# Performance work log

Measured on AMD Instinct MI355X. Metric: run time of the kernel, lower is better.

Reference implementation:

```python
import jax, jax.numpy as jnp
import numpy as np

B, N, C, H = 8, 1024, 768, 12
D = C // H  # 64


def setup_inputs() -> dict:
    key = jax.random.key(0)
    ks = jax.random.split(key, 6)
    x = jax.random.normal(ks[0], (B, N, C), dtype=jnp.float32)
    pad_mask = jnp.ones((B, N), dtype=jnp.int32)
    # params (torch Linear stored transposed; here kept as (in, out) for x @ W)
    s = 1.0 / np.sqrt(C)
    w_attn = jax.random.uniform(ks[1], (C, 3 * C), jnp.float32, -s, s)
    b_attn = jax.random.uniform(ks[2], (3 * C,), jnp.float32, -s, s)
    w_proj = jax.random.uniform(ks[3], (C, C), jnp.float32, -s, s)
    b_proj = jax.random.uniform(ks[4], (C,), jnp.float32, -s, s)
    return {"x": x, "pad_mask": pad_mask, "w_attn": w_attn,
            "b_attn": b_attn, "w_proj": w_proj, "b_proj": b_proj}


def reference(x, pad_mask, w_attn, b_attn, w_proj, b_proj):
    # qkv projection
    qkv = x @ w_attn + b_attn                      # [B,N,3C]
    q, k, v = jnp.split(qkv, 3, axis=-1)
    q = q.reshape(B, N, H, D).transpose(0, 2, 1, 3)  # [B,H,N,D]
    k = k.reshape(B, N, H, D).transpose(0, 2, 1, 3)
    v = v.reshape(B, N, H, D).transpose(0, 2, 1, 3)
    scale = 1.0 / np.sqrt(D)
    att = jnp.einsum('bhqd,bhkd->bhqk', q, k) * scale  # [B,H,N,N]
    # NOTE: original code's causal masked_fill is non-in-place and discarded,
    # so the causal mask is NOT applied. Only the pad mask (over query rows) is.
    pm = pad_mask.reshape(B, 1, N, 1)
    att = jnp.where(pm == 0, -jnp.inf, att)
    att = jax.nn.softmax(att, axis=-1)
    out = jnp.einsum('bhqk,bhkd->bhqd', att, v)     # [B,H,N,D]
    out = out.transpose(0, 2, 1, 3).reshape(B, N, C)
    # dropout layers are identity in eval mode
    return out @ w_proj + b_proj
```

## Files before the change

### kernel.cpp

```cpp
#include <hip/hip_runtime.h>
#include <hip/hip_bf16.h>

#define B_  8
#define N_  1024
#define C_  768
#define H_  12
#define D_  64
#define C3  2304
#define C2  1536

typedef unsigned short ushort_t;
typedef __attribute__((ext_vector_type(8))) short bf16x8;
typedef __attribute__((ext_vector_type(4))) float f32x4;

__device__ __forceinline__ float bf2f(ushort_t u) {
    union { unsigned int i; float f; } v;
    v.i = ((unsigned int)u) << 16;
    return v.f;
}

__device__ __forceinline__ ushort_t f2bf(float f) {
    union { float f; unsigned int i; } v;
    v.f = f;
    unsigned int x = v.i;
    if ((x & 0x7f800000u) == 0x7f800000u && (x & 0x007fffffu))
        return (ushort_t)((x >> 16) | 0x0040u);
    return (ushort_t)((x + 0x7fffu + ((x >> 16) & 1u)) >> 16);
}

__device__ __forceinline__ void st1(float* p, float v) { *p = v; }
__device__ __forceinline__ void st1(ushort_t* p, float v) { *p = f2bf(v); }

__global__ __launch_bounds__(256) void cvt_bf16(
    const float* __restrict__ X, ushort_t* __restrict__ Y, int n)
{
    int i = (blockIdx.x * 256 + threadIdx.x) * 4;
    if (i < n) {
        float4 f = *reinterpret_cast<const float4*>(X + i);
        ushort4 o;
        o.x = f2bf(f.x); o.y = f2bf(f.y); o.z = f2bf(f.z); o.w = f2bf(f.w);
        *reinterpret_cast<ushort4*>(Y + i) = o;
    }
}

__global__ __launch_bounds__(256) void transpose_to_bf16(
    const float* __restrict__ W, ushort_t* __restrict__ WT, int K, int Nn)
{
    __shared__ float t[32][33];
    const int n0 = blockIdx.x * 32, k0 = blockIdx.y * 32;
    const int tx = threadIdx.x & 31, ty = threadIdx.x >> 5;
    #pragma unroll
    for (int i = 0; i < 4; ++i) {
        const int k = ty + i * 8;
        t[k][tx] = W[(size_t)(k0 + k) * Nn + n0 + tx];
    }
    __syncthreads();
    #pragma unroll
    for (int i = 0; i < 4; ++i) {
        const int n = ty + i * 8;
        WT[(size_t)(n0 + n) * K + k0 + tx] = f2bf(t[tx][n]);
    }
}

__device__ __forceinline__ void gld_lds16(const ushort_t* g, ushort_t* lds) {
    __builtin_amdgcn_global_load_lds(
        (const __attribute__((address_space(1))) void*)g,
        (__attribute__((address_space(3))) void*)lds, 16, 0, 0);
}

template<typename TO, bool SCALEQ>
__global__ __launch_bounds__(256) void gemm_mfma(
    const ushort_t* __restrict__ A, const ushort_t* __restrict__ BT,
    const float* __restrict__ bias, TO* __restrict__ Y, int ldY,
    ushort_t* __restrict__ vtOut, int M, int K, int Nn)
{
    __shared__ ushort_t As[128 * 32];
    __shared__ ushort_t Bs[128 * 32];

    const int tid  = threadIdx.x;
    const int wave = tid >> 6;
    const int lane = tid & 63;
    const int row0 = blockIdx.y * 128;
    const int col0 = blockIdx.x * 128;
    const int wr   = (wave >> 1) * 64;
    const int wc   = (wave & 1) * 64;
    const int l15  = lane & 15;
    const int quad = lane >> 4;

    const int lrow = lane >> 2;
    const int sk   = (lane & 3) * 8;

    f32x4 acc[4][4] = {};

    for (int k0 = 0; k0 < K; k0 += 32) {
        __syncthreads();
        #pragma unroll
        for (int it = 0; it < 2; ++it) {
            const int baseRow = it * 64 + wave * 16;
            const int r = baseRow + lrow;
            gld_lds16(&A [(size_t)(row0 + r) * K + k0 + sk], &As[baseRow * 32]);
            gld_lds16(&BT[(size_t)(col0 + r) * K + k0 + sk], &Bs[baseRow * 32]);
        }
        __syncthreads();

        bf16x8 af[4], bf[4];
        #pragma unroll
        for (int i = 0; i < 4; ++i) {
            af[i] = *reinterpret_cast<const bf16x8*>(&As[(wr + i * 16 + l15) * 32 + quad * 8]);
            bf[i] = *reinterpret_cast<const bf16x8*>(&Bs[(wc + i * 16 + l15) * 32 + quad * 8]);
        }
        #pragma unroll
        for (int i = 0; i < 4; ++i)
            #pragma unroll
            for (int j = 0; j < 4; ++j)
                acc[i][j] = __builtin_amdgcn_mfma_f32_16x16x32_bf16(
                    af[i], bf[j], acc[i][j], 0, 0, 0);
    }

    const float qs = (SCALEQ && (col0 + wc) < C_) ? 0.125f : 1.0f;

    if (vtOut != nullptr && col0 >= C2) {
        #pragma unroll
        for (int i = 0; i < 4; ++i) {
            const int r0 = row0 + wr + i * 16 + quad * 4;
            const int bb = r0 >> 10;
            const int n  = r0 & 1023;
            #pragma unroll
            for (int j = 0; j < 4; ++j) {
                const int c  = col0 + wc + j * 16 + l15;
                const int cv = c - C2;
                const int hh = cv >> 6, d = cv & 63;
                const float bv = bias[c];
                ushort4 o;
                o.x = f2bf(acc[i][j][0] + bv);
                o.y = f2bf(acc[i][j][1] + bv);
                o.z = f2bf(acc[i][j][2] + bv);
                o.w = f2bf(acc[i][j][3] + bv);
                *reinterpret_cast<ushort4*>(
                    &vtOut[((size_t)(bb * H_ + hh) * D_ + d) * N_ + n]) = o;
            }
        }
    } else {
        #pragma unroll
        for (int i = 0; i < 4; ++i) {
            const int r = row0 + wr + i * 16 + quad * 4;
            #pragma unroll
            for (int j = 0; j < 4; ++j) {
                const int c = col0 + wc + j * 16 + l15;
                const float bv = bias[c];
                #pragma unroll
                for (int t = 0; t < 4; ++t)
                    st1(&Y[(size_t)(r + t) * ldY + c], (acc[i][j][t] + bv) * qs);
            }
        }
    }
}

#define LDT 72

__global__ __launch_bounds__(256) void attn_mfma(
    const ushort_t* __restrict__ qk, const ushort_t* __restrict__ vt,
    const int* __restrict__ pad_mask, ushort_t* __restrict__ y)
{
    __shared__ ushort_t Ks [64 * LDT];
    __shared__ ushort_t Vts[64 * LDT];
    __shared__ ushort_t Ps [4][32 * LDT];

    const int tid  = threadIdx.x;
    const int wave = tid >> 6;
    const int lane = tid & 63;
    const int l15  = lane & 15;
    const int quad = lane >> 4;

    const int qt = blockIdx.x & 7;
    const int h  = (blockIdx.x >> 3) % H_;
    const int b  = blockIdx.x / (8 * H_);
    const int q0 = qt * 128 + wave * 32;

    const ushort_t* qkB = qk + (size_t)b * N_ * C2;
    const ushort_t* vtB = vt + ((size_t)(b * H_ + h)) * D_ * N_;
    const int ho = h * D_;

    bf16x8 qf[2][2];
    #pragma unroll
    for (int rt = 0; rt < 2; ++rt)
        #pragma unroll
        for (int kc = 0; kc < 2; ++kc)
            qf[rt][kc] = *reinterpret_cast<const bf16x8*>(
                &qkB[(size_t)(q0 + rt * 16 + l15) * C2 + ho + kc * 32 + quad * 8]);

    int mrow[2][4];
    #pragma unroll
    for (int rt = 0; rt < 2; ++rt)
        #pragma unroll
        for (int t = 0; t < 4; ++t)
            mrow[rt][t] = pad_mask[b * N_ + q0 + rt * 16 + quad * 4 + t];

    f32x4 oacc[2][4] = {};
    float den[2][4] = {};

    const int srow = tid >> 3;
    const int scol = (tid & 7) * 8;

    for (int k0 = 0; k0 < N_; k0 += 64) {
        __syncthreads();
        #pragma unroll
        for (int half = 0; half < 2; ++half) {
            const int r = srow + half * 32;
            uint4 kv = *reinterpret_cast<const uint4*>(
                &qkB[(size_t)(k0 + r) * C2 + C_ + ho + scol]);
            uint4 vv = *reinterpret_cast<const uint4*>(
                &vtB[(size_t)r * N_ + k0 + scol]);
            *reinterpret_cast<uint4*>(&Ks [r * LDT + scol]) = kv;
            *reinterpret_cast<uint4*>(&Vts[r * LDT + scol]) = vv;
        }
        __syncthreads();

        f32x4 s[2][4] = {};
        #pragma unroll
        for (int kc = 0; kc < 2; ++kc) {
            bf16x8 kf[4];
            #pragma unroll
            for (int ct = 0; ct < 4; ++ct)
                kf[ct] = *reinterpret_cast<const bf16x8*>(
                    &Ks[(ct * 16 + l15) * LDT + kc * 32 + quad * 8]);
            #pragma unroll
            for (int rt = 0; rt < 2; ++rt)
                #pragma unroll
                for (int ct = 0; ct < 4; ++ct)
                    s[rt][ct] = __builtin_amdgcn_mfma_f32_16x16x32_bf16(
                        qf[rt][kc], kf[ct], s[rt][ct], 0, 0, 0);
        }

        ushort_t* Pw = Ps[wave];
        #pragma unroll
        for (int rt = 0; rt < 2; ++rt)
            #pragma unroll
            for (int ct = 0; ct < 4; ++ct)
                #pragma unroll
                for (int t = 0; t < 4; ++t) {
                    float p = __expf(s[rt][ct][t]);
                    unsigned u = (__float_as_uint(p) + 0x8000u) & 0xffff0000u;
                    den[rt][t] += __uint_as_float(u);
                    Pw[(rt * 16 + quad * 4 + t) * LDT + ct * 16 + l15] =
                        (ushort_t)(u >> 16);
                }

        #pragma unroll
        for (int kc = 0; kc < 2; ++kc) {
            bf16x8 pf[2], vf[4];
            #pragma unroll
            for (int rt = 0; rt < 2; ++rt)
                pf[rt] = *reinterpret_cast<const bf16x8*>(
                    &Pw[(rt * 16 + l15) * LDT + kc * 32 + quad * 8]);
            #pragma unroll
            for (int dt = 0; dt < 4; ++dt)
                vf[dt] = *reinterpret_cast<const bf16x8*>(
                    &Vts[(dt * 16 + l15) * LDT + kc * 32 + quad * 8]);
            #pragma unroll
            for (int rt = 0; rt < 2; ++rt)
                #pragma unroll
                for (int dt = 0; dt < 4; ++dt)
                    oacc[rt][dt] = __builtin_amdgcn_mfma_f32_16x16x32_bf16(
                        pf[rt], vf[dt], oacc[rt][dt], 0, 0, 0);
        }
    }

    #pragma unroll
    for (int rt = 0; rt < 2; ++rt)
        #pragma unroll
        for (int t = 0; t < 4; ++t) {
            float v = den[rt][t];
            v += __shfl_xor(v, 1);
            v += __shfl_xor(v, 2);
            v += __shfl_xor(v, 4);
            v += __shfl_xor(v, 8);
            const float inv = mrow[rt][t] ? 1.0f / v : __builtin_nanf("");
            const size_t row = (size_t)(b * N_ + q0 + rt * 16 + quad * 4 + t);
            #pragma unroll
            for (int dt = 0; dt < 4; ++dt)
                y[row * C_ + ho + dt * 16 + l15] = f2bf(oacc[rt][dt][t] * inv);
        }
}

extern "C" void kernel_launch(void* const* d_in, const int* in_sizes, int n_in,
                              void* d_out, int out_size, void* d_ws, size_t ws_size,
                              hipStream_t stream)
{
    const float* x      = (const float*)d_in[0];
    const int*   pad    = (const int*)d_in[1];
    const float* w_attn = (const float*)d_in[2];
    const float* b_attn = (const float*)d_in[3];
    const float* w_proj = (const float*)d_in[4];
    const float* b_proj = (const float*)d_in[5];
    float* out = (float*)d_out;

    ushort_t* qkb = (ushort_t*)d_ws;
    ushort_t* vtb = qkb + (size_t)B_ * N_ * C2;
    ushort_t* y   = vtb + (size_t)B_ * H_ * D_ * N_;
    ushort_t* xb  = y;
    ushort_t* wat = y + (size_t)B_ * N_ * C_;
    ushort_t* wpt = wat + (size_t)C3 * C_;

    const int M = B_ * N_;

    cvt_bf16<<<dim3((M * C_) / (256 * 4)), dim3(256), 0, stream>>>(x, xb, M * C_);
    transpose_to_bf16<<<dim3(C3 / 32, C_ / 32), dim3(256), 0, stream>>>(
        w_attn, wat, C_, C3);
    transpose_to_bf16<<<dim3(C_ / 32, C_ / 32), dim3(256), 0, stream>>>(
        w_proj, wpt, C_, C_);

    gemm_mfma<ushort_t, true><<<dim3(C3 / 128, M / 128), dim3(256), 0, stream>>>(
        xb, wat, b_attn, qkb, C2, vtb, M, C_, C3);

    attn_mfma<<<dim3(B_ * H_ * 8), dim3(256), 0, stream>>>(qkb, vtb, pad, y);

    gemm_mfma<float, false><<<dim3(C_ / 128, M / 128), dim3(256), 0, stream>>>(
        y, wpt, b_proj, out, C_, nullptr, M, C_, C_);
}
```

Measured before the change: 220.3 us.

## Double GEMM K-tile to 64 with XOR-swizzled LDS and stage attention output

The MFMA GEMM now loads 64-wide K tiles per barrier pair instead of 32, using an XOR swizzle on the 16-byte LDS slots to avoid bank conflicts on the fragment reads. This halves the number of synchronisations per GEMM and doubles LDS usage. The attention kernel's epilogue now writes normalized output into the per-wave P scratch in LDS, then stores it to global memory as 16-byte vectors instead of scattered 2-byte stores. This relies on the P buffer being free at that point and on LDT being large enough for 64 columns.

After: 219.1 us. No clear change (-0.5%).

```diff
diff --git a/kernel.cpp b/kernel.cpp
--- a/kernel.cpp
+++ b/kernel.cpp
@@ -62,6 +62,8 @@
     }
 }
 
+#define GBK 64
+
 __device__ __forceinline__ void gld_lds16(const ushort_t* g, ushort_t* lds) {
     __builtin_amdgcn_global_load_lds(
         (const __attribute__((address_space(1))) void*)g,
@@ -74,8 +76,8 @@
     const float* __restrict__ bias, TO* __restrict__ Y, int ldY,
     ushort_t* __restrict__ vtOut, int M, int K, int Nn)
 {
-    __shared__ ushort_t As[128 * 32];
-    __shared__ ushort_t Bs[128 * 32];
+    __shared__ ushort_t As[128 * GBK];
+    __shared__ ushort_t Bs[128 * GBK];
 
     const int tid  = threadIdx.x;
     const int wave = tid >> 6;
@@ -86,35 +88,42 @@
     const int wc   = (wave & 1) * 64;
     const int l15  = lane & 15;
     const int quad = lane >> 4;
-
-    const int lrow = lane >> 2;
-    const int sk   = (lane & 3) * 8;
+    const int l7   = l15 & 7;
+
+    const int srow = lane >> 3;
+    const int sg   = (lane & 7) ^ srow;
 
     f32x4 acc[4][4] = {};
 
-    for (int k0 = 0; k0 < K; k0 += 32) {
+    for (int k0 = 0; k0 < K; k0 += GBK) {
         __syncthreads();
         #pragma unroll
-        for (int it = 0; it < 2; ++it) {
-            const int baseRow = it * 64 + wave * 16;
-            const int r = baseRow + lrow;
-            gld_lds16(&A [(size_t)(row0 + r) * K + k0 + sk], &As[baseRow * 32]);
-            gld_lds16(&BT[(size_t)(col0 + r) * K + k0 + sk], &Bs[baseRow * 32]);
+        for (int it = 0; it < 4; ++it) {
+            const int baseRow = wave * 32 + it * 8;
+            const int r = baseRow + srow;
+            gld_lds16(&A [(size_t)(row0 + r) * K + k0 + sg * 8], &As[baseRow * GBK]);
+            gld_lds16(&BT[(size_t)(col0 + r) * K + k0 + sg * 8], &Bs[baseRow * GBK]);
         }
         __syncthreads();
 
-        bf16x8 af[4], bf[4];
-        #pragma unroll
-        for (int i = 0; i < 4; ++i) {
-            af[i] = *reinterpret_cast<const bf16x8*>(&As[(wr + i * 16 + l15) * 32 + quad * 8]);
-            bf[i] = *reinterpret_cast<const bf16x8*>(&Bs[(wc + i * 16 + l15) * 32 + quad * 8]);
-        }
-        #pragma unroll
-        for (int i = 0; i < 4; ++i)
-            #pragma unroll
-            for (int j = 0; j < 4; ++j)
-                acc[i][j] = __builtin_amdgcn_mfma_f32_16x16x32_bf16(
-                    af[i], bf[j], acc[i][j], 0, 0, 0);
+        #pragma unroll
+        for (int kc = 0; kc < 2; ++kc) {
+            bf16x8 af[4], bf[4];
+            #pragma unroll
+            for (int i = 0; i < 4; ++i) {
+                const int aslot = (kc * 4 + quad) ^ l7;
+                af[i] = *reinterpret_cast<const bf16x8*>(
+                    &As[(wr + i * 16 + l15) * GBK + aslot * 8]);
+                bf[i] = *reinterpret_cast<const bf16x8*>(
+                    &Bs[(wc + i * 16 + l15) * GBK + aslot * 8]);
+            }
+            #pragma unroll
+            for (int i = 0; i < 4; ++i)
+                #pragma unroll
+                for (int j = 0; j < 4; ++j)
+                    acc[i][j] = __builtin_amdgcn_mfma_f32_16x16x32_bf16(
+                        af[i], bf[j], acc[i][j], 0, 0, 0);
+        }
     }
 
     const float qs = (SCALEQ && (col0 + wc) < C_) ? 0.125f : 1.0f;
@@ -266,6 +275,7 @@
         }
     }
 
+    ushort_t* Pw = Ps[wave];
     #pragma unroll
     for (int rt = 0; rt < 2; ++rt)
         #pragma unroll
@@ -276,11 +286,21 @@
             v += __shfl_xor(v, 4);
             v += __shfl_xor(v, 8);
             const float inv = mrow[rt][t] ? 1.0f / v : __builtin_nanf("");
-            const size_t row = (size_t)(b * N_ + q0 + rt * 16 + quad * 4 + t);
+            const int row = rt * 16 + quad * 4 + t;
             #pragma unroll
             for (int dt = 0; dt < 4; ++dt)
-                y[row * C_ + ho + dt * 16 + l15] = f2bf(oacc[rt][dt][t] * inv);
-        }
+                Pw[row * LDT + dt * 16 + l15] = f2bf(oacc[rt][dt][t] * inv);
+        }
+    {
+        const int orow = lane >> 1;
+        const int ocol = (lane & 1) * 32;
+        const size_t gr = (size_t)(b * N_ + q0 + orow) * C_ + ho + ocol;
+        #pragma unroll
+        for (int i2 = 0; i2 < 4; ++i2) {
+            uint4 w = *reinterpret_cast<const uint4*>(&Pw[orow * LDT + ocol + i2 * 8]);
+            *reinterpret_cast<uint4*>(&y[gr + i2 * 8]) = w;
+        }
+    }
 }
 
 extern "C" void kernel_launch(void* const* d_in, const int* in_sizes, int n_in,
```
